# Kernel optimization log

Measured on AMD Instinct MI355X. Metric: run time of the kernel, lower is better.

## Reference

```python
import jax, jax.numpy as jnp
import numpy as np

NUM_HEADS = 16
HEAD_DIM = 64
ROPE_BASE = 160000.0


def _rope_tables(seq_len, head_dim):
    inv_freq = 1.0 / (ROPE_BASE ** (jnp.arange(0, head_dim, 2, dtype=jnp.float32) / head_dim))
    freqs = jnp.arange(seq_len, dtype=jnp.float32)[:, None] * inv_freq[None, :]  # [S, hd/2]
    return jnp.cos(freqs)[None, None], jnp.sin(freqs)[None, None]  # [1,1,S,hd/2]


def _apply_rope(x, cos, sin):
    # x: [B, nh, S, hd]; split-half rotation as in the torch module
    x1, x2 = jnp.split(x, 2, axis=-1)
    return jnp.concatenate([x1 * cos - x2 * sin, x2 * cos + x1 * sin], axis=-1)


def setup_inputs() -> dict:
    key = jax.random.key(0)
    k1, k2, k3 = jax.random.split(key, 3)
    B, S, H = 2, 2048, 1024
    hidden_states = jax.random.normal(k1, (B, S, H), dtype=jnp.float32)
    # additive causal mask: 0 for allowed, -1e9 for future positions
    causal = jnp.tril(jnp.ones((S, S), dtype=bool))
    attention_mask = jnp.where(causal, 0.0, -1e9).astype(jnp.float32)[None, None]
    Wqkv = jax.random.normal(k2, (H, 3 * H), dtype=jnp.float32) * (H ** -0.5)
    Wo = jax.random.normal(k3, (H, H), dtype=jnp.float32) * (H ** -0.5)
    return {"hidden_states": hidden_states, "attention_mask": attention_mask, "Wqkv": Wqkv, "Wo": Wo}


def reference(hidden_states, attention_mask, Wqkv, Wo):
    B, S, H = hidden_states.shape
    nh, hd = NUM_HEADS, HEAD_DIM
    scale = hd ** -0.5

    qkv = hidden_states @ Wqkv                                   # [B,S,3H]
    qkv = qkv.reshape(B, S, 3, nh, hd).transpose(2, 0, 3, 1, 4)  # [3,B,nh,S,hd]
    q, k, v = qkv[0], qkv[1], qkv[2]

    cos, sin = _rope_tables(S, hd)
    q = _apply_rope(q, cos, sin)
    k = _apply_rope(k, cos, sin)

    scores = jnp.einsum('bhqd,bhkd->bhqk', q, k) * scale + attention_mask
    attn = jax.nn.softmax(scores, axis=-1)
    out = jnp.einsum('bhqk,bhkd->bhqd', attn, v)                 # [B,nh,S,hd]
    out = out.transpose(0, 2, 1, 3).reshape(B, S, H)
    return out @ Wo
```

## Files before the change

kernel.cpp:

```cpp
#include <hip/hip_runtime.h>
#include <hip/hip_bf16.h>

typedef __bf16 bf16x8 __attribute__((ext_vector_type(8)));
typedef float f32x4 __attribute__((ext_vector_type(4)));
typedef unsigned short u16;

__device__ __forceinline__ u16 f2bf(float f) {
    union { float f; unsigned u; } x{f};
    unsigned r = x.u + 0x7fffu + ((x.u >> 16) & 1u);
    return (u16)(r >> 16);
}
__device__ __forceinline__ unsigned pk2(float a, float b) {
    union { float f; unsigned u; } x{a}, y{b};
    return ((x.u + 0x8000u) >> 16) | ((y.u + 0x8000u) & 0xffff0000u);
}
__device__ __forceinline__ float ex2(float x) { return __builtin_amdgcn_exp2f(x); }
__device__ __forceinline__ f32x4 zero4() { f32x4 z = {0.f, 0.f, 0.f, 0.f}; return z; }

typedef const __attribute__((address_space(1))) unsigned int* gp1_t;
typedef __attribute__((address_space(3))) unsigned int* lp3_t;
__device__ __forceinline__ void async16(const u16* g, u16* l) {
    __builtin_amdgcn_global_load_lds((gp1_t)g, (lp3_t)l, 16, 0, 0);
}

__global__ void __launch_bounds__(256) prep(const float* __restrict__ hs,
                                            u16* __restrict__ Xb,
                                            const float* __restrict__ Wqkv,
                                            u16* __restrict__ Wqkvt,
                                            const float* __restrict__ Wo,
                                            u16* __restrict__ Wot,
                                            float* __restrict__ cosT,
                                            float* __restrict__ sinT) {
    __shared__ float tile[32][33];
    const int blk = blockIdx.x, t = threadIdx.x;
    if (blk < 4096) {
        int i = (blk * 256 + t) * 4;
        float4 v = *(const float4*)(hs + i);
        ushort4 o;
        o.x = f2bf(v.x); o.y = f2bf(v.y); o.z = f2bf(v.z); o.w = f2bf(v.w);
        *(ushort4*)(Xb + i) = o;
    } else if (blk < 8192) {
        const float* W; u16* Wt; int N, bx, by;
        if (blk < 7168) { int bid = blk - 4096; W = Wqkv; Wt = Wqkvt; N = 3072; bx = bid % 96; by = bid / 96; }
        else            { int bid = blk - 7168; W = Wo;   Wt = Wot;   N = 1024; bx = bid % 32; by = bid / 32; }
        const int K = 1024;
        int tx = t & 31, ty = t >> 5;
        int n0 = bx * 32, k0 = by * 32;
#pragma unroll
        for (int i = 0; i < 32; i += 8)
            tile[ty + i][tx] = W[(size_t)(k0 + ty + i) * N + n0 + tx];
        __syncthreads();
#pragma unroll
        for (int i = 0; i < 32; i += 8)
            Wt[(size_t)(n0 + ty + i) * K + k0 + tx] = f2bf(tile[tx][ty + i]);
    } else {
        int idx = (blk - 8192) * 256 + t;
        int d = idx & 31, s = idx >> 5;
        float inv = expf(-(float)d * 0.374466538f);
        float th = (float)s * inv;
        cosT[idx] = cosf(th);
        sinT[idx] = sinf(th);
    }
}

struct GemmCtx {
    f32x4 acc[4][4];
    int m16, q4, wm, wn;
};
template <int KDIM>
__device__ __forceinline__ void gemm_loop(const u16* __restrict__ A,
                                          const u16* __restrict__ Bt,
                                          int bm, int bn, GemmCtx& cx,
                                          u16* As, u16* Bs) {
    const int t = threadIdx.x;
    const int lane = t & 63, w = t >> 6;
    cx.wm = w >> 1; cx.wn = w & 1;
    cx.m16 = lane & 15; cx.q4 = lane >> 4;

    const int lrow = lane >> 2;
    const int kchunk = (lane & 3) ^ ((lane >> 3) & 3);
    const u16* Ag = A + (size_t)(bm * 128 + w * 32 + lrow) * KDIM + kchunk * 8;
    const u16* Bg = Bt + (size_t)(bn * 128 + w * 32 + lrow) * KDIM + kchunk * 8;
    const int l0 = (w * 32) * 32;
    const int l1 = (w * 32 + 16) * 32;
    const int kswz = (cx.q4 ^ ((cx.m16 >> 1) & 3)) * 8;

#pragma unroll
    for (int i = 0; i < 4; i++)
#pragma unroll
        for (int j = 0; j < 4; j++) cx.acc[i][j] = zero4();

    constexpr int NT = KDIM / 32;
    async16(Ag, As + l0);
    async16(Ag + 16 * KDIM, As + l1);
    async16(Bg, Bs + l0);
    async16(Bg + 16 * KDIM, Bs + l1);

#pragma unroll 1
    for (int tt = 0; tt < NT; ++tt) {
        const int co = (tt & 1) * 4096;
        if (tt + 1 < NT) {
            const int no = 4096 - co;
            const int k0 = (tt + 1) * 32;
            async16(Ag + k0, As + no + l0);
            async16(Ag + 16 * KDIM + k0, As + no + l1);
            async16(Bg + k0, Bs + no + l0);
            async16(Bg + 16 * KDIM + k0, Bs + no + l1);
            asm volatile("s_waitcnt vmcnt(4)" ::: "memory");
        } else {
            asm volatile("s_waitcnt vmcnt(0)" ::: "memory");
        }
        __builtin_amdgcn_s_barrier();
        asm volatile("" ::: "memory");
        __builtin_amdgcn_sched_barrier(0);

        bf16x8 af[4], bf[4];
#pragma unroll
        for (int i = 0; i < 4; i++)
            af[i] = *(const bf16x8*)&As[co + (cx.wm * 64 + i * 16 + cx.m16) * 32 + kswz];
#pragma unroll
        for (int j = 0; j < 4; j++)
            bf[j] = *(const bf16x8*)&Bs[co + (cx.wn * 64 + j * 16 + cx.m16) * 32 + kswz];
#pragma unroll
        for (int i = 0; i < 4; i++)
#pragma unroll
            for (int j = 0; j < 4; j++)
                cx.acc[i][j] = __builtin_amdgcn_mfma_f32_16x16x32_bf16(af[i], bf[j], cx.acc[i][j], 0, 0, 0);

        asm volatile("" ::: "memory");
        __builtin_amdgcn_sched_barrier(0);
        __builtin_amdgcn_s_barrier();
    }
}

struct GemmCtx2 {
    f32x4 acc[4][8];
    int m16, q4, wm;
};
template <int KDIM>
__device__ __forceinline__ void gemm_loop2(const u16* __restrict__ A,
                                           const u16* __restrict__ Bt,
                                           int bm, int bn, GemmCtx2& cx,
                                           u16* As, u16* Bs) {
    const int t = threadIdx.x;
    const int lane = t & 63, w = t >> 6;
    cx.wm = w;
    cx.m16 = lane & 15; cx.q4 = lane >> 4;

    const int lrow = lane >> 2;
    const int kchunk = (lane & 3) ^ ((lane >> 3) & 3);
    const u16* Ag = A + (size_t)(bm * 128 + w * 64 + lrow) * KDIM + kchunk * 8;
    const u16* Bg = Bt + (size_t)(bn * 128 + w * 64 + lrow) * KDIM + kchunk * 8;
    const int lb = (w * 64) * 32;
    const int kswz = (cx.q4 ^ ((cx.m16 >> 1) & 3)) * 8;

#pragma unroll
    for (int i = 0; i < 4; i++)
#pragma unroll
        for (int j = 0; j < 8; j++) cx.acc[i][j] = zero4();

    constexpr int NT = KDIM / 32;
#pragma unroll
    for (int c = 0; c < 4; c++) {
        async16(Ag + c * 16 * KDIM, As + lb + c * 16 * 32);
        async16(Bg + c * 16 * KDIM, Bs + lb + c * 16 * 32);
    }

#pragma unroll 1
    for (int tt = 0; tt < NT; ++tt) {
        const int co = (tt & 1) * 4096;
        if (tt + 1 < NT) {
            const int no = 4096 - co;
            const int k0 = (tt + 1) * 32;
#pragma unroll
            for (int c = 0; c < 4; c++) {
                async16(Ag + k0 + c * 16 * KDIM, As + no + lb + c * 16 * 32);
                async16(Bg + k0 + c * 16 * KDIM, Bs + no + lb + c * 16 * 32);
            }
            asm volatile("s_waitcnt vmcnt(8)" ::: "memory");
        } else {
            asm volatile("s_waitcnt vmcnt(0)" ::: "memory");
        }
        __builtin_amdgcn_s_barrier();
        asm volatile("" ::: "memory");
        __builtin_amdgcn_sched_barrier(0);

        bf16x8 af[4], bf[8];
#pragma unroll
        for (int i = 0; i < 4; i++)
            af[i] = *(const bf16x8*)&As[co + (cx.wm * 64 + i * 16 + cx.m16) * 32 + kswz];
#pragma unroll
        for (int j = 0; j < 8; j++)
            bf[j] = *(const bf16x8*)&Bs[co + (j * 16 + cx.m16) * 32 + kswz];
#pragma unroll
        for (int i = 0; i < 4; i++)
#pragma unroll
            for (int j = 0; j < 8; j++)
                cx.acc[i][j] = __builtin_amdgcn_mfma_f32_16x16x32_bf16(af[i], bf[j], cx.acc[i][j], 0, 0, 0);

        asm volatile("" ::: "memory");
        __builtin_amdgcn_sched_barrier(0);
        __builtin_amdgcn_s_barrier();
    }
}

__global__ void __launch_bounds__(128, 2) gemm_qkv(const u16* __restrict__ A,
                                                   const u16* __restrict__ Bt,
                                                   const float* __restrict__ cosT,
                                                   const float* __restrict__ sinT,
                                                   u16* __restrict__ Q,
                                                   u16* __restrict__ Kd,
                                                   u16* __restrict__ Vt) {
    __shared__ __align__(16) u16 As[2 * 128 * 32];
    __shared__ __align__(16) u16 Bs[2 * 128 * 32];
    GemmCtx2 cx;
    const int hw = blockIdx.x;
    const int orig = (hw & 7) * 96 + (hw >> 3);
    const int bm = orig / 24, bn = orig % 24;
    gemm_loop2<1024>(A, Bt, bm, bn, cx, As, Bs);
    const int m16 = cx.m16, q4 = cx.q4;

    const int colblk = bn * 128;
    const int type = colblk >> 10;
    const int h0 = (colblk & 1023) >> 6;
    const int rbase = bm * 128 + cx.wm * 64;

    if (type == 2) {
#pragma unroll
        for (int i = 0; i < 4; i++) {
            int s0 = rbase + i * 16 + q4 * 4;
            int b = s0 >> 11, sl = s0 & 2047;
#pragma unroll
            for (int j = 0; j < 8; j++) {
                int h = h0 + (j >> 2);
                int d = (j & 3) * 16 + m16;
                size_t ob = (size_t)(b * 16 + h) * 64 * 2048;
                ushort4 o;
                o.x = f2bf(cx.acc[i][j][0]);
                o.y = f2bf(cx.acc[i][j][1]);
                o.z = f2bf(cx.acc[i][j][2]);
                o.w = f2bf(cx.acc[i][j][3]);
                *(ushort4*)&Vt[ob + (size_t)d * 2048 + sl] = o;
            }
        }
    } else {
        u16* dst = (type == 0) ? Q : Kd;
        const float qs = (type == 0) ? 0.1803368801f  : 1.0f;
#pragma unroll
        for (int i = 0; i < 4; i++)
#pragma unroll
            for (int rr = 0; rr < 4; rr++) {
                int r = rbase + i * 16 + q4 * 4 + rr;
                int b = r >> 11, s = r & 2047;
#pragma unroll
                for (int hh = 0; hh < 2; hh++) {
                    size_t ob = ((size_t)((b * 16 + h0 + hh) * 2048 + s)) * 64;
#pragma unroll
                    for (int j2 = 0; j2 < 2; j2++) {
                        int d = j2 * 16 + m16;
                        float cs = cosT[s * 32 + d];
                        float sn = sinT[s * 32 + d];
                        float x1 = cx.acc[i][hh * 4 + j2][rr];
                        float x2 = cx.acc[i][hh * 4 + j2 + 2][rr];
                        dst[ob + d]      = f2bf((x1 * cs - x2 * sn) * qs);
                        dst[ob + d + 32] = f2bf((x2 * cs + x1 * sn) * qs);
                    }
                }
            }
    }
}

__global__ void __launch_bounds__(256) gemm_out(const u16* __restrict__ A,
                                                const u16* __restrict__ Bt,
                                                float* __restrict__ C) {
    __shared__ __align__(16) u16 As[2 * 128 * 32];
    __shared__ __align__(16) u16 Bs[2 * 128 * 32];
    GemmCtx cx;
    const int bm = blockIdx.y, bn = blockIdx.x;
    gemm_loop<1024>(A, Bt, bm, bn, cx, As, Bs);
    const int N = 1024;
#pragma unroll
    for (int i = 0; i < 4; i++)
#pragma unroll
        for (int j = 0; j < 4; j++)
#pragma unroll
            for (int rr = 0; rr < 4; rr++) {
                int row = bm * 128 + cx.wm * 64 + i * 16 + cx.q4 * 4 + rr;
                int col = bn * 128 + cx.wn * 64 + j * 16 + cx.m16;
                C[(size_t)row * N + col] = cx.acc[i][j][rr];
            }
}

__global__ void __launch_bounds__(512) attn_kernel(const u16* __restrict__ Q,
                                                   const u16* __restrict__ Kg_,
                                                   const u16* __restrict__ Vtg_,
                                                   u16* __restrict__ O) {
    __shared__ __align__(16) u16 Ks[2][64][72];
    __shared__ __align__(16) u16 Vs[2][64][72];
    __shared__ __align__(16) u16 Pt[8][16][72];
    const int t = threadIdx.x, w = t >> 6;
    const int m16 = t & 15, q4 = (t & 63) >> 4;
    const int bx = blockIdx.x, bh = blockIdx.y;
    const size_t base = (size_t)bh * 2048 * 64;
    const int b = bh >> 4, h = bh & 15;
    const int skey = t >> 3, sc = (t & 7) * 8;

#pragma unroll 1
    for (int ph = 0; ph < 2; ph++) {
        const int st = ph ? (15 - bx) : bx;
        const int qrow = st * 128 + w * 16 + m16;
        const u16* Qg = Q + base + (size_t)qrow * 64;
        bf16x8 qf0 = *(const bf16x8*)(Qg + q4 * 8);
        bf16x8 qf1 = *(const bf16x8*)(Qg + 32 + q4 * 8);

        f32x4 occ[4];
#pragma unroll
        for (int dc = 0; dc < 4; dc++) occ[dc] = zero4();
        float li = 0.f;

        const int jtmax = 2 * st + 1;
        const int jd = 2 * st + (w >> 2);

        const u16* Kb0 = Kg_ + base + skey * 64 + sc;
        const u16* Vt0 = Vtg_ + base + (size_t)skey * 2048 + sc;
        uint4 ka = *(const uint4*)(Kb0);
        uint4 va = *(const uint4*)(Vt0);

#pragma unroll 1
        for (int jt = 0; jt <= jtmax; jt++) {
            const int bi = jt & 1;
            *(uint4*)&Ks[bi][skey][sc] = ka;
            *(uint4*)&Vs[bi][skey][sc] = va;
            if (jt < jtmax) {
                ka = *(const uint4*)(Kb0 + (size_t)(jt + 1) * 4096);
                va = *(const uint4*)(Vt0 + (size_t)(jt + 1) * 64);
            }
            __syncthreads();

            if (jt <= jd) {
                f32x4 stv[4];
#pragma unroll
                for (int c = 0; c < 4; c++) stv[c] = zero4();
#pragma unroll
                for (int c = 0; c < 4; c++) {
                    bf16x8 kf0 = *(const bf16x8*)&Ks[bi][c * 16 + m16][q4 * 8];
                    bf16x8 kf1 = *(const bf16x8*)&Ks[bi][c * 16 + m16][32 + q4 * 8];
                    stv[c] = __builtin_amdgcn_mfma_f32_16x16x32_bf16(kf0, qf0, stv[c], 0, 0, 0);
                    stv[c] = __builtin_amdgcn_mfma_f32_16x16x32_bf16(kf1, qf1, stv[c], 0, 0, 0);
                }

                float pv[4][4];
#pragma unroll
                for (int c = 0; c < 4; c++)
#pragma unroll
                    for (int rr = 0; rr < 4; rr++) pv[c][rr] = stv[c][rr];
                if (jt == jd) {
                    const int ql = qrow - 64 * jt;
#pragma unroll
                    for (int c = 0; c < 4; c++)
#pragma unroll
                        for (int rr = 0; rr < 4; rr++)
                            if (c * 16 + q4 * 4 + rr > ql) pv[c][rr] = -1e30f;
                }

#pragma unroll
                for (int c = 0; c < 4; c++) {
                    float p0 = ex2(pv[c][0] - 24.f);
                    float p1 = ex2(pv[c][1] - 24.f);
                    float p2 = ex2(pv[c][2] - 24.f);
                    float p3 = ex2(pv[c][3] - 24.f);
                    li += (p0 + p1) + (p2 + p3);
                    *(uint2*)&Pt[w][m16][c * 16 + q4 * 4] = make_uint2(pk2(p0, p1), pk2(p2, p3));
                }

#pragma unroll
                for (int ks = 0; ks < 2; ks++) {
                    bf16x8 pf = *(const bf16x8*)&Pt[w][m16][ks * 32 + q4 * 8];
#pragma unroll
                    for (int dc = 0; dc < 4; dc++) {
                        bf16x8 vf = *(const bf16x8*)&Vs[bi][dc * 16 + m16][ks * 32 + q4 * 8];
                        occ[dc] = __builtin_amdgcn_mfma_f32_16x16x32_bf16(vf, pf, occ[dc], 0, 0, 0);
                    }
                }
            }
        }

        li += __shfl_xor(li, 16);
        li += __shfl_xor(li, 32);
        float rli = 1.0f / li;
        u16* Op = O + ((size_t)(b * 2048 + qrow)) * 1024 + h * 64 + q4 * 4;
#pragma unroll
        for (int dc = 0; dc < 4; dc++) {
            ushort4 o;
            o.x = f2bf(occ[dc][0] * rli);
            o.y = f2bf(occ[dc][1] * rli);
            o.z = f2bf(occ[dc][2] * rli);
            o.w = f2bf(occ[dc][3] * rli);
            *(ushort4*)(Op + dc * 16) = o;
        }
        __syncthreads();
    }
}

extern "C" void kernel_launch(void* const* d_in, const int* in_sizes, int n_in,
                              void* d_out, int out_size, void* d_ws, size_t ws_size,
                              hipStream_t stream) {
    const float* hs   = (const float*)d_in[0];
    const float* Wqkv = (const float*)d_in[2];
    const float* Wo   = (const float*)d_in[3];
    float* out = (float*)d_out;

    const int BS = 4096;
    const int H = 1024, N3 = 3072;
    const int SH = 32 * 2048 * 64;

    u16* Xb    = (u16*)d_ws;
    u16* Wqkvt = Xb + (size_t)BS * H;
    u16* Wot   = Wqkvt + (size_t)N3 * H;
    u16* Qb    = Wot + (size_t)H * H;
    u16* Kb    = Qb + SH;
    u16* Vtb   = Kb + SH;
    u16* AOb   = Vtb + SH;
    float* cosT = (float*)(AOb + (size_t)BS * H);
    float* sinT = cosT + 2048 * 32;

    prep<<<8448, 256, 0, stream>>>(hs, Xb, Wqkv, Wqkvt, Wo, Wot, cosT, sinT);

    gemm_qkv<<<768, 128, 0, stream>>>(Xb, Wqkvt, cosT, sinT, Qb, Kb, Vtb);

    attn_kernel<<<dim3(8, 32), 512, 0, stream>>>(Qb, Kb, Vtb, AOb);

    gemm_out<<<dim3(H / 128, BS / 128), 256, 0, stream>>>(AOb, Wot, out);
}
```

Measured before the change: 189.2 us.

## Triple-buffer GEMM shared-memory tiles and drop trailing barrier

Both GEMM loops move from double to triple buffering of the A/B shared-memory tiles. Two K-slices are prefetched up front, and each iteration issues the load for slice tt+2 after the single barrier. This lets the second per-iteration s_barrier be removed while keeping loads two stages ahead. The cost is 50% more LDS per block (48KB), which may reduce occupancy, especially for gemm_qkv with launch bounds of 2 blocks.

```diff
diff --git a/kernel.cpp b/kernel.cpp
--- a/kernel.cpp
+++ b/kernel.cpp
@@ -95,23 +95,28 @@
     async16(Ag + 16 * KDIM, As + l1);
     async16(Bg, Bs + l0);
     async16(Bg + 16 * KDIM, Bs + l1);
-
+    async16(Ag + 32, As + 4096 + l0);
+    async16(Ag + 16 * KDIM + 32, As + 4096 + l1);
+    async16(Bg + 32, Bs + 4096 + l0);
+    async16(Bg + 16 * KDIM + 32, Bs + 4096 + l1);
+
+    int co = 0, po = 2 * 4096;
 #pragma unroll 1
     for (int tt = 0; tt < NT; ++tt) {
-        const int co = (tt & 1) * 4096;
         if (tt + 1 < NT) {
-            const int no = 4096 - co;
-            const int k0 = (tt + 1) * 32;
-            async16(Ag + k0, As + no + l0);
-            async16(Ag + 16 * KDIM + k0, As + no + l1);
-            async16(Bg + k0, Bs + no + l0);
-            async16(Bg + 16 * KDIM + k0, Bs + no + l1);
             asm volatile("s_waitcnt vmcnt(4)" ::: "memory");
         } else {
             asm volatile("s_waitcnt vmcnt(0)" ::: "memory");
         }
         __builtin_amdgcn_s_barrier();
-        asm volatile("" ::: "memory");
+        __builtin_amdgcn_sched_barrier(0);
+        if (tt + 2 < NT) {
+            const int k0 = (tt + 2) * 32;
+            async16(Ag + k0, As + po + l0);
+            async16(Ag + 16 * KDIM + k0, As + po + l1);
+            async16(Bg + k0, Bs + po + l0);
+            async16(Bg + 16 * KDIM + k0, Bs + po + l1);
+        }
         __builtin_amdgcn_sched_barrier(0);
 
         bf16x8 af[4], bf[4];
@@ -129,7 +134,8 @@
 
         asm volatile("" ::: "memory");
         __builtin_amdgcn_sched_barrier(0);
-        __builtin_amdgcn_s_barrier();
+        co += 4096; if (co == 12288) co = 0;
+        po += 4096; if (po == 12288) po = 0;
     }
 }
 
@@ -165,24 +171,30 @@
         async16(Ag + c * 16 * KDIM, As + lb + c * 16 * 32);
         async16(Bg + c * 16 * KDIM, Bs + lb + c * 16 * 32);
     }
-
+#pragma unroll
+    for (int c = 0; c < 4; c++) {
+        async16(Ag + 32 + c * 16 * KDIM, As + 4096 + lb + c * 16 * 32);
+        async16(Bg + 32 + c * 16 * KDIM, Bs + 4096 + lb + c * 16 * 32);
+    }
+
+    int co = 0, po = 2 * 4096;
 #pragma unroll 1
     for (int tt = 0; tt < NT; ++tt) {
-        const int co = (tt & 1) * 4096;
         if (tt + 1 < NT) {
-            const int no = 4096 - co;
-            const int k0 = (tt + 1) * 32;
-#pragma unroll
-            for (int c = 0; c < 4; c++) {
-                async16(Ag + k0 + c * 16 * KDIM, As + no + lb + c * 16 * 32);
-                async16(Bg + k0 + c * 16 * KDIM, Bs + no + lb + c * 16 * 32);
-            }
             asm volatile("s_waitcnt vmcnt(8)" ::: "memory");
         } else {
             asm volatile("s_waitcnt vmcnt(0)" ::: "memory");
         }
         __builtin_amdgcn_s_barrier();
-        asm volatile("" ::: "memory");
+        __builtin_amdgcn_sched_barrier(0);
+        if (tt + 2 < NT) {
+            const int k0 = (tt + 2) * 32;
+#pragma unroll
+            for (int c = 0; c < 4; c++) {
+                async16(Ag + k0 + c * 16 * KDIM, As + po + lb + c * 16 * 32);
+                async16(Bg + k0 + c * 16 * KDIM, Bs + po + lb + c * 16 * 32);
+            }
+        }
         __builtin_amdgcn_sched_barrier(0);
 
         bf16x8 af[4], bf[8];
@@ -200,7 +212,8 @@
 
         asm volatile("" ::: "memory");
         __builtin_amdgcn_sched_barrier(0);
-        __builtin_amdgcn_s_barrier();
+        co += 4096; if (co == 12288) co = 0;
+        po += 4096; if (po == 12288) po = 0;
     }
 }
 
@@ -211,8 +224,8 @@
                                                    u16* __restrict__ Q,
                                                    u16* __restrict__ Kd,
                                                    u16* __restrict__ Vt) {
-    __shared__ __align__(16) u16 As[2 * 128 * 32];
-    __shared__ __align__(16) u16 Bs[2 * 128 * 32];
+    __shared__ __align__(16) u16 As[3 * 128 * 32];
+    __shared__ __align__(16) u16 Bs[3 * 128 * 32];
     GemmCtx2 cx;
     const int hw = blockIdx.x;
     const int orig = (hw & 7) * 96 + (hw >> 3);
@@ -273,8 +286,8 @@
 __global__ void __launch_bounds__(256) gemm_out(const u16* __restrict__ A,
                                                 const u16* __restrict__ Bt,
                                                 float* __restrict__ C) {
-    __shared__ __align__(16) u16 As[2 * 128 * 32];
-    __shared__ __align__(16) u16 Bs[2 * 128 * 32];
+    __shared__ __align__(16) u16 As[3 * 128 * 32];
+    __shared__ __align__(16) u16 Bs[3 * 128 * 32];
     GemmCtx cx;
     const int bm = blockIdx.y, bn = blockIdx.x;
     gemm_loop<1024>(A, Bt, bm, bn, cx, As, Bs);
```

Measured after the change: 190.6 us. Within noise of the previous version (+0.7%).
